# Kernel tuning notes

Measured on AMD Instinct MI355X. Metric: run time of the kernel, lower is better.

## Reference

```python
import jax, jax.numpy as jnp
import numpy as np

N_NODES = 100000
N_EDGES = 1600000
D_FEAT = 64
NUM_ITERS = 10  # init kwarg num_iterations


def setup_inputs() -> dict:
    key = jax.random.key(0)
    k1, k2, k3 = jax.random.split(key, 3)
    x = jax.random.normal(k1, (N_NODES, D_FEAT), dtype=jnp.float32)
    edge_index = jax.random.randint(k2, (2, N_EDGES), 0, N_NODES, dtype=jnp.int32)
    mask = jax.random.randint(k3, (N_NODES,), 0, 2, dtype=jnp.int32) > 0  # known-feature nodes
    return {"x": x, "edge_index": edge_index, "mask": mask}


def reference(x, edge_index, mask):
    row, col = edge_index[0], edge_index[1]
    # symmetric normalization: deg from scatter_add over col, D^{-1/2} A D^{-1/2}
    deg = jax.ops.segment_sum(jnp.ones((edge_index.shape[1],), x.dtype), col,
                              num_segments=N_NODES)
    deg_inv_sqrt = jnp.where(deg > 0, jax.lax.rsqrt(deg), 0.0)  # inf -> 0 as in masked_fill_
    w = deg_inv_sqrt[row] * deg_inv_sqrt[col]  # [E]

    # initialize: zeros everywhere, known rows copied from x
    out = jnp.where(mask[:, None], x, 0.0)
    for _ in range(NUM_ITERS):
        # SpMM: (A @ out)[i] = sum_{e: row_e=i} w_e * out[col_e]
        out = jax.ops.segment_sum(w[:, None] * out[col], row, num_segments=N_NODES)
        # masked reset: known rows are clamped back to x
        out = jnp.where(mask[:, None], x, out)
    return out
```

## Files before the change

kernel.cpp:

```cpp
#include <hip/hip_runtime.h>
#include <stdint.h>


typedef unsigned short bf16_t;
typedef unsigned int u32;

__device__ __forceinline__ float bf2f(u32 u) {
  union { u32 i; float f; } v;
  v.i = u << 16;
  return v.f;
}
__device__ __forceinline__ u32 f2bf(float f) {
  union { float f; u32 i; } v;
  v.f = f;
  u32 u = v.i;
  return (u + 0x7FFFu + ((u >> 16) & 1u)) >> 16;
}

__device__ __forceinline__ bool mask_at(const void* m, int i, int byteFlag) {
  return byteFlag ? (((const uint8_t*)m)[i] != 0) : (((const int*)m)[i] != 0);
}

__global__ void k_detect_mask(const uint8_t* m, int n, int* flag) {
  __shared__ int isByte, anyAligned;
  if (threadIdx.x == 0) { isByte = 0; anyAligned = 0; }
  __syncthreads();
  int nb = n < 4096 ? n : 4096;
  for (int i = threadIdx.x; i < nb; i += blockDim.x) {
    uint8_t v = m[i];
    if (v) {
      if (i & 3) atomicOr(&isByte, 1);
      else       atomicOr(&anyAligned, 1);
    }
  }
  __syncthreads();
  if (threadIdx.x == 0) *flag = (isByte || !anyAligned) ? 1 : 0;
}

__global__ void k_fused_preproc(const int* __restrict__ row, const int* __restrict__ col,
                                int E, const void* __restrict__ mask,
                                const int* __restrict__ flag, int CAP,
                                int* __restrict__ deg_col, int* __restrict__ cursor,
                                int* __restrict__ csr) {
  int e = blockIdx.x * blockDim.x + threadIdx.x;
  if (e >= E) return;
  int fl = *flag;
  int r = row[e], c = col[e];
  atomicAdd(&deg_col[c], 1);
  if (!mask_at(mask, r, fl)) {
    int pos = atomicAdd(&cursor[r], 1);
    if (pos < CAP) csr[r * CAP + pos] = c;
  }
}

__global__ void k_dinv(const int* __restrict__ deg_col, float* __restrict__ dinv, int N) {
  int i = blockIdx.x * blockDim.x + threadIdx.x;
  if (i >= N) return;
  int d = deg_col[i];
  dinv[i] = d > 0 ? rsqrtf((float)d) : 0.0f;
}

__global__ void k_init_state(const float* __restrict__ x, const float* __restrict__ dinv,
                             const void* __restrict__ mask, const int* __restrict__ flag,
                             bf16_t* __restrict__ b0, bf16_t* __restrict__ b1, int total) {
  int i = blockIdx.x * blockDim.x + threadIdx.x;
  if (i >= total) return;
  int n = i >> 6;
  if (mask_at(mask, n, *flag)) {
    bf16_t v = (bf16_t)f2bf(dinv[n] * x[i]);
    b0[i] = v;
    b1[i] = v;
  } else {
    b0[i] = 0;
  }
}

__global__ void __launch_bounds__(256)
k_spmm_mid(const int* __restrict__ csr, const int* __restrict__ cursor, int CAP,
           const bf16_t* __restrict__ src, const float* __restrict__ dinv,
           const void* __restrict__ mask, const int* __restrict__ flag,
           bf16_t* __restrict__ dst, int N) {
  int wid = blockIdx.x * (blockDim.x >> 6) + (threadIdx.x >> 6);
  int lane = threadIdx.x & 63;
  if (wid >= N) return;
  if (mask_at(mask, wid, *flag)) return;
  int cnt = cursor[wid];
  if (cnt > CAP) cnt = CAP;
  int colv = (lane < cnt) ? csr[wid * CAP + lane] : 0;
  int g = lane >> 3, li = lane & 7;
  float a0 = 0.f, a1 = 0.f, a2 = 0.f, a3 = 0.f, a4 = 0.f, a5 = 0.f, a6 = 0.f, a7 = 0.f;
  int kmax = (cnt + 7) >> 3;
  for (int k = 0; k < kmax; ++k) {
    int ei = (k << 3) + g;
    int c = __shfl(colv, ei, 64);
    if (ei < cnt) {
      const uint4* pp = (const uint4*)(src + (((size_t)c) << 6) + (li << 3));
      uint4 v = *pp;
      a0 += bf2f(v.x & 0xffffu); a1 += bf2f(v.x >> 16);
      a2 += bf2f(v.y & 0xffffu); a3 += bf2f(v.y >> 16);
      a4 += bf2f(v.z & 0xffffu); a5 += bf2f(v.z >> 16);
      a6 += bf2f(v.w & 0xffffu); a7 += bf2f(v.w >> 16);
    }
  }
  a0 += __shfl_xor(a0, 8, 64); a0 += __shfl_xor(a0, 16, 64); a0 += __shfl_xor(a0, 32, 64);
  a1 += __shfl_xor(a1, 8, 64); a1 += __shfl_xor(a1, 16, 64); a1 += __shfl_xor(a1, 32, 64);
  a2 += __shfl_xor(a2, 8, 64); a2 += __shfl_xor(a2, 16, 64); a2 += __shfl_xor(a2, 32, 64);
  a3 += __shfl_xor(a3, 8, 64); a3 += __shfl_xor(a3, 16, 64); a3 += __shfl_xor(a3, 32, 64);
  a4 += __shfl_xor(a4, 8, 64); a4 += __shfl_xor(a4, 16, 64); a4 += __shfl_xor(a4, 32, 64);
  a5 += __shfl_xor(a5, 8, 64); a5 += __shfl_xor(a5, 16, 64); a5 += __shfl_xor(a5, 32, 64);
  a6 += __shfl_xor(a6, 8, 64); a6 += __shfl_xor(a6, 16, 64); a6 += __shfl_xor(a6, 32, 64);
  a7 += __shfl_xor(a7, 8, 64); a7 += __shfl_xor(a7, 16, 64); a7 += __shfl_xor(a7, 32, 64);
  if (g == 0) {
    float di = dinv[wid];
    float s = di * di;
    uint4 o;
    o.x = f2bf(s * a0) | (f2bf(s * a1) << 16);
    o.y = f2bf(s * a2) | (f2bf(s * a3) << 16);
    o.z = f2bf(s * a4) | (f2bf(s * a5) << 16);
    o.w = f2bf(s * a6) | (f2bf(s * a7) << 16);
    *(uint4*)(dst + (((size_t)wid) << 6) + (li << 3)) = o;
  }
}

__global__ void __launch_bounds__(256)
k_spmm_fin(const int* __restrict__ csr, const int* __restrict__ cursor, int CAP,
           const bf16_t* __restrict__ src, const float* __restrict__ dinv,
           const float* __restrict__ x, const void* __restrict__ mask,
           const int* __restrict__ flag, float* __restrict__ out, int N) {
  int wid = blockIdx.x * (blockDim.x >> 6) + (threadIdx.x >> 6);
  int lane = threadIdx.x & 63;
  if (wid >= N) return;
  int base = (wid << 6) + lane;
  if (mask_at(mask, wid, *flag)) { out[base] = x[base]; return; }
  int cnt = cursor[wid];
  if (cnt > CAP) cnt = CAP;
  int colv = (lane < cnt) ? csr[wid * CAP + lane] : 0;
  int g = lane >> 3, li = lane & 7;
  float a0 = 0.f, a1 = 0.f, a2 = 0.f, a3 = 0.f, a4 = 0.f, a5 = 0.f, a6 = 0.f, a7 = 0.f;
  int kmax = (cnt + 7) >> 3;
  for (int k = 0; k < kmax; ++k) {
    int ei = (k << 3) + g;
    int c = __shfl(colv, ei, 64);
    if (ei < cnt) {
      const uint4* pp = (const uint4*)(src + (((size_t)c) << 6) + (li << 3));
      uint4 v = *pp;
      a0 += bf2f(v.x & 0xffffu); a1 += bf2f(v.x >> 16);
      a2 += bf2f(v.y & 0xffffu); a3 += bf2f(v.y >> 16);
      a4 += bf2f(v.z & 0xffffu); a5 += bf2f(v.z >> 16);
      a6 += bf2f(v.w & 0xffffu); a7 += bf2f(v.w >> 16);
    }
  }
  a0 += __shfl_xor(a0, 8, 64); a0 += __shfl_xor(a0, 16, 64); a0 += __shfl_xor(a0, 32, 64);
  a1 += __shfl_xor(a1, 8, 64); a1 += __shfl_xor(a1, 16, 64); a1 += __shfl_xor(a1, 32, 64);
  a2 += __shfl_xor(a2, 8, 64); a2 += __shfl_xor(a2, 16, 64); a2 += __shfl_xor(a2, 32, 64);
  a3 += __shfl_xor(a3, 8, 64); a3 += __shfl_xor(a3, 16, 64); a3 += __shfl_xor(a3, 32, 64);
  a4 += __shfl_xor(a4, 8, 64); a4 += __shfl_xor(a4, 16, 64); a4 += __shfl_xor(a4, 32, 64);
  a5 += __shfl_xor(a5, 8, 64); a5 += __shfl_xor(a5, 16, 64); a5 += __shfl_xor(a5, 32, 64);
  a6 += __shfl_xor(a6, 8, 64); a6 += __shfl_xor(a6, 16, 64); a6 += __shfl_xor(a6, 32, 64);
  a7 += __shfl_xor(a7, 8, 64); a7 += __shfl_xor(a7, 16, 64); a7 += __shfl_xor(a7, 32, 64);
  if (g == 0) {
    float di = dinv[wid];
    float* po = out + (((size_t)wid) << 6) + (li << 3);
    float4 o0, o1;
    o0.x = di * a0; o0.y = di * a1; o0.z = di * a2; o0.w = di * a3;
    o1.x = di * a4; o1.y = di * a5; o1.z = di * a6; o1.w = di * a7;
    *(float4*)po = o0;
    *(float4*)(po + 4) = o1;
  }
}

extern "C" void kernel_launch(void* const* d_in, const int* in_sizes, int n_in,
                              void* d_out, int out_size, void* d_ws, size_t ws_size,
                              hipStream_t stream) {
  const float* x   = (const float*)d_in[0];
  const int*   ei  = (const int*)d_in[1];
  const void*  msk = d_in[2];
  const int N = in_sizes[2];
  const int E = in_sizes[1] / 2;
  const int* row = ei;
  const int* col = ei + E;

  size_t fixedBytes = 2 * (((size_t)N * 64 * 2 + 255) & ~(size_t)255)
                    + 3 * (((size_t)N * 4 + 255) & ~(size_t)255)
                    + 512;
  int CAP = 64;
  if (fixedBytes + (size_t)N * 64 * 4 > ws_size) CAP = 48;
  if (CAP == 48 && fixedBytes + (size_t)N * 48 * 4 > ws_size) CAP = 32;

  char* p = (char*)d_ws;
  auto alloc = [&](size_t bytes) -> char* {
    char* r = p;
    p += (bytes + 255) & ~(size_t)255;
    return r;
  };
  bf16_t* b0   = (bf16_t*)alloc((size_t)N * 64 * 2);
  bf16_t* b1   = (bf16_t*)alloc((size_t)N * 64 * 2);
  int*    degc = (int*)alloc((size_t)N * 4);
  float*  dinv = (float*)alloc((size_t)N * 4);
  int*    cursor = (int*)alloc((size_t)N * 4);
  int*    flag = (int*)alloc(256);
  int*    csr  = (int*)alloc((size_t)N * CAP * 4);
  (void)n_in; (void)out_size;

  hipMemsetAsync(degc, 0, (size_t)N * 4, stream);
  hipMemsetAsync(cursor, 0, (size_t)N * 4, stream);

  const int tb = 256;
  k_detect_mask<<<1, 1024, 0, stream>>>((const uint8_t*)msk, N, flag);
  k_fused_preproc<<<(E + tb - 1) / tb, tb, 0, stream>>>(row, col, E, msk, flag, CAP,
                                                        degc, cursor, csr);
  k_dinv<<<(N + tb - 1) / tb, tb, 0, stream>>>(degc, dinv, N);

  int totalElems = N * 64;
  k_init_state<<<(totalElems + tb - 1) / tb, tb, 0, stream>>>(x, dinv, msk, flag, b0, b1,
                                                              totalElems);

  int wavesPerBlock = tb / 64;
  int grid = (N + wavesPerBlock - 1) / wavesPerBlock;
  bf16_t* a = b0;
  bf16_t* b = b1;
  for (int it = 0; it < 9; ++it) {
    k_spmm_mid<<<grid, tb, 0, stream>>>(csr, cursor, CAP, a, dinv, msk, flag, b, N);
    bf16_t* t = a; a = b; b = t;
  }
  k_spmm_fin<<<grid, tb, 0, stream>>>(csr, cursor, CAP, a, dinv, x, msk, flag,
                                      (float*)d_out, N);
}
```

Baseline: 452.4 us.

## Compact unknown-node worklist and use persistent SpMM waves with software prefetch

```diff
diff --git a/kernel.cpp b/kernel.cpp
--- a/kernel.cpp
+++ b/kernel.cpp
@@ -53,119 +53,149 @@
   }
 }
 
-__global__ void k_dinv(const int* __restrict__ deg_col, float* __restrict__ dinv, int N) {
+__global__ void k_dinv_wlist(const int* __restrict__ deg_col, float* __restrict__ dinv,
+                             const void* __restrict__ mask, const int* __restrict__ flag,
+                             int* __restrict__ wlist, int* __restrict__ n_un, int N) {
   int i = blockIdx.x * blockDim.x + threadIdx.x;
   if (i >= N) return;
   int d = deg_col[i];
   dinv[i] = d > 0 ? rsqrtf((float)d) : 0.0f;
+  if (!mask_at(mask, i, *flag)) {
+    int pos = atomicAdd(n_un, 1);
+    wlist[pos] = i;
+  }
 }
 
 __global__ void k_init_state(const float* __restrict__ x, const float* __restrict__ dinv,
                              const void* __restrict__ mask, const int* __restrict__ flag,
-                             bf16_t* __restrict__ b0, bf16_t* __restrict__ b1, int total) {
+                             bf16_t* __restrict__ b0, bf16_t* __restrict__ b1,
+                             float* __restrict__ out, int total) {
   int i = blockIdx.x * blockDim.x + threadIdx.x;
   if (i >= total) return;
   int n = i >> 6;
   if (mask_at(mask, n, *flag)) {
-    bf16_t v = (bf16_t)f2bf(dinv[n] * x[i]);
+    float xv = x[i];
+    bf16_t v = (bf16_t)f2bf(dinv[n] * xv);
     b0[i] = v;
     b1[i] = v;
+    out[i] = xv;
   } else {
     b0[i] = 0;
   }
 }
 
+#define ROW_GATHER_REDUCE()                                                        \
+  int colv = (lane < cnt) ? craw : 0;                                              \
+  float a0 = 0.f, a1 = 0.f, a2 = 0.f, a3 = 0.f,                                    \
+        a4 = 0.f, a5 = 0.f, a6 = 0.f, a7 = 0.f;                                    \
+  int kmax = (cnt + 7) >> 3;                                                       \
+  uint4 vc = make_uint4(0, 0, 0, 0);                                               \
+  {                                                                                \
+    int c0 = __shfl(colv, g, 64);                                                  \
+    if (g < cnt)                                                                   \
+      vc = *(const uint4*)(src + (((size_t)c0) << 6) + (li << 3));                 \
+  }                                                                                \
+  for (int k = 0; k < kmax; ++k) {                                                 \
+    uint4 vn = make_uint4(0, 0, 0, 0);                                             \
+    int ei_n = ((k + 1) << 3) + g;                                                 \
+    int c_n = __shfl(colv, ei_n & 63, 64);                                         \
+    if (k + 1 < kmax && ei_n < cnt)                                                \
+      vn = *(const uint4*)(src + (((size_t)c_n) << 6) + (li << 3));                \
+    a0 += bf2f(vc.x & 0xffffu); a1 += bf2f(vc.x >> 16);                            \
+    a2 += bf2f(vc.y & 0xffffu); a3 += bf2f(vc.y >> 16);                            \
+    a4 += bf2f(vc.z & 0xffffu); a5 += bf2f(vc.z >> 16);                            \
+    a6 += bf2f(vc.w & 0xffffu); a7 += bf2f(vc.w >> 16);                            \
+    vc = vn;                                                                       \
+  }                                                                                \
+  a0 += __shfl_xor(a0, 8, 64); a0 += __shfl_xor(a0, 16, 64); a0 += __shfl_xor(a0, 32, 64); \
+  a1 += __shfl_xor(a1, 8, 64); a1 += __shfl_xor(a1, 16, 64); a1 += __shfl_xor(a1, 32, 64); \
+  a2 += __shfl_xor(a2, 8, 64); a2 += __shfl_xor(a2, 16, 64); a2 += __shfl_xor(a2, 32, 64); \
+  a3 += __shfl_xor(a3, 8, 64); a3 += __shfl_xor(a3, 16, 64); a3 += __shfl_xor(a3, 32, 64); \
+  a4 += __shfl_xor(a4, 8, 64); a4 += __shfl_xor(a4, 16, 64); a4 += __shfl_xor(a4, 32, 64); \
+  a5 += __shfl_xor(a5, 8, 64); a5 += __shfl_xor(a5, 16, 64); a5 += __shfl_xor(a5, 32, 64); \
+  a6 += __shfl_xor(a6, 8, 64); a6 += __shfl_xor(a6, 16, 64); a6 += __shfl_xor(a6, 32, 64); \
+  a7 += __shfl_xor(a7, 8, 64); a7 += __shfl_xor(a7, 16, 64); a7 += __shfl_xor(a7, 32, 64);
+
 __global__ void __launch_bounds__(256)
-k_spmm_mid(const int* __restrict__ csr, const int* __restrict__ cursor, int CAP,
+k_spmm_mid(const int* __restrict__ wlist, const int* __restrict__ n_un,
+           const int* __restrict__ csr, const int* __restrict__ cursor, int CAP,
            const bf16_t* __restrict__ src, const float* __restrict__ dinv,
-           const void* __restrict__ mask, const int* __restrict__ flag,
-           bf16_t* __restrict__ dst, int N) {
-  int wid = blockIdx.x * (blockDim.x >> 6) + (threadIdx.x >> 6);
+           bf16_t* __restrict__ dst) {
+  int wpb = blockDim.x >> 6;
+  int stride = gridDim.x * wpb;
   int lane = threadIdx.x & 63;
-  if (wid >= N) return;
-  if (mask_at(mask, wid, *flag)) return;
-  int cnt = cursor[wid];
-  if (cnt > CAP) cnt = CAP;
-  int colv = (lane < cnt) ? csr[wid * CAP + lane] : 0;
   int g = lane >> 3, li = lane & 7;
-  float a0 = 0.f, a1 = 0.f, a2 = 0.f, a3 = 0.f, a4 = 0.f, a5 = 0.f, a6 = 0.f, a7 = 0.f;
-  int kmax = (cnt + 7) >> 3;
-  for (int k = 0; k < kmax; ++k) {
-    int ei = (k << 3) + g;
-    int c = __shfl(colv, ei, 64);
-    if (ei < cnt) {
-      const uint4* pp = (const uint4*)(src + (((size_t)c) << 6) + (li << 3));
-      uint4 v = *pp;
-      a0 += bf2f(v.x & 0xffffu); a1 += bf2f(v.x >> 16);
-      a2 += bf2f(v.y & 0xffffu); a3 += bf2f(v.y >> 16);
-      a4 += bf2f(v.z & 0xffffu); a5 += bf2f(v.z >> 16);
-      a6 += bf2f(v.w & 0xffffu); a7 += bf2f(v.w >> 16);
-    }
-  }
-  a0 += __shfl_xor(a0, 8, 64); a0 += __shfl_xor(a0, 16, 64); a0 += __shfl_xor(a0, 32, 64);
-  a1 += __shfl_xor(a1, 8, 64); a1 += __shfl_xor(a1, 16, 64); a1 += __shfl_xor(a1, 32, 64);
-  a2 += __shfl_xor(a2, 8, 64); a2 += __shfl_xor(a2, 16, 64); a2 += __shfl_xor(a2, 32, 64);
-  a3 += __shfl_xor(a3, 8, 64); a3 += __shfl_xor(a3, 16, 64); a3 += __shfl_xor(a3, 32, 64);
-  a4 += __shfl_xor(a4, 8, 64); a4 += __shfl_xor(a4, 16, 64); a4 += __shfl_xor(a4, 32, 64);
-  a5 += __shfl_xor(a5, 8, 64); a5 += __shfl_xor(a5, 16, 64); a5 += __shfl_xor(a5, 32, 64);
-  a6 += __shfl_xor(a6, 8, 64); a6 += __shfl_xor(a6, 16, 64); a6 += __shfl_xor(a6, 32, 64);
-  a7 += __shfl_xor(a7, 8, 64); a7 += __shfl_xor(a7, 16, 64); a7 += __shfl_xor(a7, 32, 64);
-  if (g == 0) {
-    float di = dinv[wid];
-    float s = di * di;
-    uint4 o;
-    o.x = f2bf(s * a0) | (f2bf(s * a1) << 16);
-    o.y = f2bf(s * a2) | (f2bf(s * a3) << 16);
-    o.z = f2bf(s * a4) | (f2bf(s * a5) << 16);
-    o.w = f2bf(s * a6) | (f2bf(s * a7) << 16);
-    *(uint4*)(dst + (((size_t)wid) << 6) + (li << 3)) = o;
+  int n = *n_un;
+  int i = blockIdx.x * wpb + (threadIdx.x >> 6);
+  if (i >= n) return;
+  int rid = wlist[i];
+  int cnt = cursor[rid]; if (cnt > CAP) cnt = CAP;
+  int craw = csr[rid * CAP + lane];
+  float di = dinv[rid];
+  while (true) {
+    int inext = i + stride;
+    bool have_next = inext < n;
+    int rid2 = 0, cnt2 = 0, craw2 = 0;
+    float di2 = 0.f;
+    if (have_next) {
+      rid2 = wlist[inext];
+      cnt2 = cursor[rid2]; if (cnt2 > CAP) cnt2 = CAP;
+      craw2 = csr[rid2 * CAP + lane];
+      di2 = dinv[rid2];
+    }
+    ROW_GATHER_REDUCE()
+    if (g == 0) {
+      float s = di * di;
+      uint4 o;
+      o.x = f2bf(s * a0) | (f2bf(s * a1) << 16);
+      o.y = f2bf(s * a2) | (f2bf(s * a3) << 16);
+      o.z = f2bf(s * a4) | (f2bf(s * a5) << 16);
+      o.w = f2bf(s * a6) | (f2bf(s * a7) << 16);
+      *(uint4*)(dst + (((size_t)rid) << 6) + (li << 3)) = o;
+    }
+    if (!have_next) break;
+    i = inext; rid = rid2; cnt = cnt2; craw = craw2; di = di2;
   }
 }
 
 __global__ void __launch_bounds__(256)
-k_spmm_fin(const int* __restrict__ csr, const int* __restrict__ cursor, int CAP,
+k_spmm_fin(const int* __restrict__ wlist, const int* __restrict__ n_un,
+           const int* __restrict__ csr, const int* __restrict__ cursor, int CAP,
            const bf16_t* __restrict__ src, const float* __restrict__ dinv,
-           const float* __restrict__ x, const void* __restrict__ mask,
-           const int* __restrict__ flag, float* __restrict__ out, int N) {
-  int wid = blockIdx.x * (blockDim.x >> 6) + (threadIdx.x >> 6);
+           float* __restrict__ out) {
+  int wpb = blockDim.x >> 6;
+  int stride = gridDim.x * wpb;
   int lane = threadIdx.x & 63;
-  if (wid >= N) return;
-  int base = (wid << 6) + lane;
-  if (mask_at(mask, wid, *flag)) { out[base] = x[base]; return; }
-  int cnt = cursor[wid];
-  if (cnt > CAP) cnt = CAP;
-  int colv = (lane < cnt) ? csr[wid * CAP + lane] : 0;
   int g = lane >> 3, li = lane & 7;
-  float a0 = 0.f, a1 = 0.f, a2 = 0.f, a3 = 0.f, a4 = 0.f, a5 = 0.f, a6 = 0.f, a7 = 0.f;
-  int kmax = (cnt + 7) >> 3;
-  for (int k = 0; k < kmax; ++k) {
-    int ei = (k << 3) + g;
-    int c = __shfl(colv, ei, 64);
-    if (ei < cnt) {
-      const uint4* pp = (const uint4*)(src + (((size_t)c) << 6) + (li << 3));
-      uint4 v = *pp;
-      a0 += bf2f(v.x & 0xffffu); a1 += bf2f(v.x >> 16);
-      a2 += bf2f(v.y & 0xffffu); a3 += bf2f(v.y >> 16);
-      a4 += bf2f(v.z & 0xffffu); a5 += bf2f(v.z >> 16);
-      a6 += bf2f(v.w & 0xffffu); a7 += bf2f(v.w >> 16);
-    }
-  }
-  a0 += __shfl_xor(a0, 8, 64); a0 += __shfl_xor(a0, 16, 64); a0 += __shfl_xor(a0, 32, 64);
-  a1 += __shfl_xor(a1, 8, 64); a1 += __shfl_xor(a1, 16, 64); a1 += __shfl_xor(a1, 32, 64);
-  a2 += __shfl_xor(a2, 8, 64); a2 += __shfl_xor(a2, 16, 64); a2 += __shfl_xor(a2, 32, 64);
-  a3 += __shfl_xor(a3, 8, 64); a3 += __shfl_xor(a3, 16, 64); a3 += __shfl_xor(a3, 32, 64);
-  a4 += __shfl_xor(a4, 8, 64); a4 += __shfl_xor(a4, 16, 64); a4 += __shfl_xor(a4, 32, 64);
-  a5 += __shfl_xor(a5, 8, 64); a5 += __shfl_xor(a5, 16, 64); a5 += __shfl_xor(a5, 32, 64);
-  a6 += __shfl_xor(a6, 8, 64); a6 += __shfl_xor(a6, 16, 64); a6 += __shfl_xor(a6, 32, 64);
-  a7 += __shfl_xor(a7, 8, 64); a7 += __shfl_xor(a7, 16, 64); a7 += __shfl_xor(a7, 32, 64);
-  if (g == 0) {
-    float di = dinv[wid];
-    float* po = out + (((size_t)wid) << 6) + (li << 3);
-    float4 o0, o1;
-    o0.x = di * a0; o0.y = di * a1; o0.z = di * a2; o0.w = di * a3;
-    o1.x = di * a4; o1.y = di * a5; o1.z = di * a6; o1.w = di * a7;
-    *(float4*)po = o0;
-    *(float4*)(po + 4) = o1;
+  int n = *n_un;
+  int i = blockIdx.x * wpb + (threadIdx.x >> 6);
+  if (i >= n) return;
+  int rid = wlist[i];
+  int cnt = cursor[rid]; if (cnt > CAP) cnt = CAP;
+  int craw = csr[rid * CAP + lane];
+  float di = dinv[rid];
+  while (true) {
+    int inext = i + stride;
+    bool have_next = inext < n;
+    int rid2 = 0, cnt2 = 0, craw2 = 0;
+    float di2 = 0.f;
+    if (have_next) {
+      rid2 = wlist[inext];
+      cnt2 = cursor[rid2]; if (cnt2 > CAP) cnt2 = CAP;
+      craw2 = csr[rid2 * CAP + lane];
+      di2 = dinv[rid2];
+    }
+    ROW_GATHER_REDUCE()
+    if (g == 0) {
+      float* po = out + (((size_t)rid) << 6) + (li << 3);
+      float4 o0, o1;
+      o0.x = di * a0; o0.y = di * a1; o0.z = di * a2; o0.w = di * a3;
+      o1.x = di * a4; o1.y = di * a5; o1.z = di * a6; o1.w = di * a7;
+      *(float4*)po = o0;
+      *(float4*)(po + 4) = o1;
+    }
+    if (!have_next) break;
+    i = inext; rid = rid2; cnt = cnt2; craw = craw2; di = di2;
   }
 }
 
@@ -181,8 +211,8 @@
   const int* col = ei + E;
 
   size_t fixedBytes = 2 * (((size_t)N * 64 * 2 + 255) & ~(size_t)255)
-                    + 3 * (((size_t)N * 4 + 255) & ~(size_t)255)
-                    + 512;
+                    + 4 * (((size_t)N * 4 + 255) & ~(size_t)255)
+                    + 1024;
   int CAP = 64;
   if (fixedBytes + (size_t)N * 64 * 4 > ws_size) CAP = 48;
   if (CAP == 48 && fixedBytes + (size_t)N * 48 * 4 > ws_size) CAP = 32;
@@ -193,36 +223,38 @@
     p += (bytes + 255) & ~(size_t)255;
     return r;
   };
-  bf16_t* b0   = (bf16_t*)alloc((size_t)N * 64 * 2);
-  bf16_t* b1   = (bf16_t*)alloc((size_t)N * 64 * 2);
-  int*    degc = (int*)alloc((size_t)N * 4);
-  float*  dinv = (float*)alloc((size_t)N * 4);
+  bf16_t* b0     = (bf16_t*)alloc((size_t)N * 64 * 2);
+  bf16_t* b1     = (bf16_t*)alloc((size_t)N * 64 * 2);
+  int*    degc   = (int*)alloc((size_t)N * 4);
+  float*  dinv   = (float*)alloc((size_t)N * 4);
   int*    cursor = (int*)alloc((size_t)N * 4);
-  int*    flag = (int*)alloc(256);
-  int*    csr  = (int*)alloc((size_t)N * CAP * 4);
+  int*    wlist  = (int*)alloc((size_t)N * 4);
+  int*    flag   = (int*)alloc(256);
+  int*    n_un   = (int*)alloc(256);
+  int*    csr    = (int*)alloc((size_t)N * CAP * 4);
   (void)n_in; (void)out_size;
 
   hipMemsetAsync(degc, 0, (size_t)N * 4, stream);
   hipMemsetAsync(cursor, 0, (size_t)N * 4, stream);
+  hipMemsetAsync(n_un, 0, 4, stream);
 
   const int tb = 256;
   k_detect_mask<<<1, 1024, 0, stream>>>((const uint8_t*)msk, N, flag);
   k_fused_preproc<<<(E + tb - 1) / tb, tb, 0, stream>>>(row, col, E, msk, flag, CAP,
                                                         degc, cursor, csr);
-  k_dinv<<<(N + tb - 1) / tb, tb, 0, stream>>>(degc, dinv, N);
+  k_dinv_wlist<<<(N + tb - 1) / tb, tb, 0, stream>>>(degc, dinv, msk, flag, wlist, n_un, N);
 
   int totalElems = N * 64;
   k_init_state<<<(totalElems + tb - 1) / tb, tb, 0, stream>>>(x, dinv, msk, flag, b0, b1,
-                                                              totalElems);
-
-  int wavesPerBlock = tb / 64;
-  int grid = (N + wavesPerBlock - 1) / wavesPerBlock;
+                                                              (float*)d_out, totalElems);
+
+  const int PB = 2048;
   bf16_t* a = b0;
   bf16_t* b = b1;
   for (int it = 0; it < 9; ++it) {
-    k_spmm_mid<<<grid, tb, 0, stream>>>(csr, cursor, CAP, a, dinv, msk, flag, b, N);
+    k_spmm_mid<<<PB, tb, 0, stream>>>(wlist, n_un, csr, cursor, CAP, a, dinv, b);
     bf16_t* t = a; a = b; b = t;
   }
-  k_spmm_fin<<<grid, tb, 0, stream>>>(csr, cursor, CAP, a, dinv, x, msk, flag,
-                                      (float*)d_out, N);
-}
+  k_spmm_fin<<<PB, tb, 0, stream>>>(wlist, n_un, csr, cursor, CAP, a, dinv,
+                                    (float*)d_out);
+}
```

After: 377.1 us, median of 2. -16.6%, faster.
